# Optimization experiments

Measured on AMD Instinct MI355X. Metric: run time of the kernel, lower is better.

The kernel has to match this reference:

```python
import jax, jax.numpy as jnp
import numpy as np

BATCH, N, NX, NU, NY = 64, 4096, 128, 32, 32


def setup_inputs() -> dict:
    key = jax.random.key(0)
    k1, k2, k3, k4, k5 = jax.random.split(key, 5)
    # A scaled to spectral radius ~0.9 so the recurrence is stable (module has is_stable()).
    A = jax.random.normal(k1, (NX, NX), jnp.float32) * (0.9 / np.sqrt(NX).astype(np.float32))
    B = jax.random.normal(k2, (NX, NU), jnp.float32) * (1.0 / np.sqrt(NU).astype(np.float32))
    C = jax.random.normal(k3, (NY, NX), jnp.float32) * (1.0 / np.sqrt(NX).astype(np.float32))
    D = jax.random.normal(k4, (NY, NU), jnp.float32) * (1.0 / np.sqrt(NU).astype(np.float32))
    d = jax.random.normal(k5, (BATCH, N, NU, 1), jnp.float32)
    return {"d": d, "A": A, "B": B, "C": C, "D": D}


def reference(d, A, B, C, D):
    # d: [batch, N, nu, 1]. LTI recurrence: x_{k+1} = A x_k + B u_k ; y_k = C x_k + D u_k, x_0 = 0.
    u = jnp.swapaxes(d[..., 0], 0, 1)  # [N, batch, nu] time-major for scan
    x0 = jnp.zeros((d.shape[0], A.shape[0]), d.dtype)  # [batch, nx]

    def step(x, uk):
        y = x @ C.T + uk @ D.T          # [batch, ny] uses pre-update state x_k
        x_next = x @ A.T + uk @ B.T     # [batch, nx]
        return x_next, (y, x)

    xN, (ys, xs) = jax.lax.scan(step, x0, u)
    y = jnp.swapaxes(ys, 0, 1)[..., None]                      # [batch, N, ny, 1]
    x = jnp.swapaxes(xs, 0, 1)                                 # [batch, N, nx] = x_0..x_{N-1}
    x = jnp.concatenate([x, xN[:, None]], axis=1)[..., None]   # [batch, N+1, nx, 1]
    return y, (x,)
```

## Files before the change

### kernel.cpp

```cpp
#include <hip/hip_runtime.h>
#include <stdint.h>
#include <stddef.h>

typedef short s8v   __attribute__((ext_vector_type(8)));
typedef float f32x4 __attribute__((ext_vector_type(4)));

union BF8 { s8v v; unsigned short u[8]; };

__device__ __forceinline__ float bf16_f(unsigned short h) {
  unsigned u = ((unsigned)h) << 16;
  return __builtin_bit_cast(float, u);
}
__device__ __forceinline__ void split_trunc(float x, unsigned short &h, unsigned short &l) {
  unsigned u = __builtin_bit_cast(unsigned, x);
  h = (unsigned short)(u >> 16);
  float hi = __builtin_bit_cast(float, u & 0xFFFF0000u);
  float r = x - hi;
  l = (unsigned short)(__builtin_bit_cast(unsigned, r) >> 16);
}
__device__ __forceinline__ f32x4 mfma16(s8v a, s8v b, f32x4 c) {
  return __builtin_amdgcn_mfma_f32_16x16x32_bf16(a, b, c, 0, 0, 0);
}
__device__ __forceinline__ void split8(f32x4 a, f32x4 b, s8v &h, s8v &l) {
  BF8 hh, ll;
  #pragma unroll
  for (int i = 0; i < 4; ++i) { split_trunc(a[i], hh.u[i], ll.u[i]); split_trunc(b[i], hh.u[4 + i], ll.u[4 + i]); }
  h = hh.v; l = ll.v;
}

#define BATCH 64
#define NN    4096
#define NX    128
#define NU    32
#define NY    32
#define LPAD  132
#define CH    32
#define CPB   128

#define OFF_AH   0
#define OFF_AL   32768
#define OFF_BH   65536
#define OFF_BL   73728
#define OFF_CH   81920
#define OFF_CL   90112
#define OFF_DH   98304
#define OFF_DL   100352
#define OFF_A2H  102400
#define OFF_A2L  135168
#define OFF_ABH  167936
#define OFF_ABL  176128
#define OFF_G1H  184320
#define OFF_G1L  217088
#define OFF_G2H  249856
#define OFF_G2L  282624
#define OFF_G3H  315392
#define OFF_G3L  348160
#define OFF_P0   380928
#define OFF_P1   446464
#define OFF_V    512000
#define OFF_S    4706304
#define OFF_UH   8900608
#define OFF_UL   25677824

__global__ void k_prep(const float* __restrict__ A, const float* __restrict__ B,
                       const float* __restrict__ C, const float* __restrict__ D,
                       const float* __restrict__ d,
                       float* __restrict__ P, unsigned short* A2h, unsigned short* A2l,
                       unsigned short* Ah, unsigned short* Al,
                       unsigned short* Bh, unsigned short* Bl,
                       unsigned short* Ch, unsigned short* Cl,
                       unsigned short* Dh, unsigned short* Dl,
                       unsigned short* ABh, unsigned short* ABl,
                       unsigned short* Uh, unsigned short* Ul) {
  const int blk = blockIdx.x;
  if (blk >= 180) {
    const size_t i0 = ((size_t)(blk - 180) * 256 + threadIdx.x) * 8;
    f32x4 a = *(const f32x4*)(d + i0);
    f32x4 b = *(const f32x4*)(d + i0 + 4);
    s8v h, l; split8(a, b, h, l);
    *(s8v*)(Uh + i0) = h;
    *(s8v*)(Ul + i0) = l;
    return;
  }
  int gid = blk * 256 + threadIdx.x;
  if (blk < 64) {
    int row = gid >> 7, col = gid & 127;
    const float* xr = A + row * 128;
    float a0 = 0.f, a1 = 0.f;
    #pragma unroll 8
    for (int k = 0; k < 128; k += 2) {
      a0 = fmaf(xr[k],     A[k * 128 + col],       a0);
      a1 = fmaf(xr[k + 1], A[(k + 1) * 128 + col], a1);
    }
    float acc = a0 + a1;
    P[gid] = acc;
    unsigned short h, l; split_trunc(acc, h, l);
    A2h[gid] = h; A2l[gid] = l;
  } else if (blk < 164) {
    int idx = gid - 16384;
    unsigned short h, l;
    if (idx < 16384)      { split_trunc(A[idx], h, l); Ah[idx] = h; Al[idx] = l; }
    else if (idx < 20480) { int i = idx - 16384; split_trunc(B[i], h, l); Bh[i] = h; Bl[i] = l; }
    else if (idx < 24576) { int i = idx - 20480; split_trunc(C[i], h, l); Ch[i] = h; Cl[i] = l; }
    else if (idx < 25600) { int i = idx - 24576; split_trunc(D[i], h, l); Dh[i] = h; Dl[i] = l; }
  } else {
    int i = gid - 41984;
    int row = i >> 5, col = i & 31;
    float acc = 0.f;
    #pragma unroll 8
    for (int k = 0; k < 128; ++k) acc = fmaf(A[row * 128 + k], B[k * 32 + col], acc);
    unsigned short h, l; split_trunc(acc, h, l);
    ABh[i] = h; ABl[i] = l;
  }
}

__global__ void k_mm128(const float* __restrict__ X, const float* __restrict__ Y,
                        float* __restrict__ Z, unsigned short* Zh, unsigned short* Zl,
                        int writeBF) {
  int gid = blockIdx.x * 256 + threadIdx.x;
  int row = gid >> 7, col = gid & 127;
  const float* xr = X + row * 128;
  float a0 = 0.f, a1 = 0.f;
  #pragma unroll 8
  for (int k = 0; k < 128; k += 2) {
    a0 = fmaf(xr[k],     Y[k * 128 + col],       a0);
    a1 = fmaf(xr[k + 1], Y[(k + 1) * 128 + col], a1);
  }
  float acc = a0 + a1;
  Z[gid] = acc;
  if (writeBF) { unsigned short h, l; split_trunc(acc, h, l); Zh[gid] = h; Zl[gid] = l; }
}

__global__ __launch_bounds__(256, 2) void k_pass1(
    const unsigned short* __restrict__ Uh, const unsigned short* __restrict__ Ul,
    const unsigned short* __restrict__ A2h, const unsigned short* __restrict__ A2l,
    const unsigned short* __restrict__ ABh, const unsigned short* __restrict__ ABl,
    const unsigned short* __restrict__ Bh,  const unsigned short* __restrict__ Bl,
    float* __restrict__ vout) {
  __shared__ unsigned short Xh[2][16][LPAD];
  __shared__ unsigned short Xl[2][16][LPAD];
  const int tid = threadIdx.x;
  const int w = tid >> 6, l = tid & 63, q = l >> 4, m = l & 15;
  const int g = blockIdx.x;

  s8v fA2h[2][4], fA2l[2][4], fABh[2], fABl[2], fBh[2], fBl[2];
  #pragma unroll
  for (int t2 = 0; t2 < 2; ++t2) {
    const int n = (2 * w + t2) * 16 + m;
    #pragma unroll
    for (int kt = 0; kt < 4; ++kt) {
      const int k0 = kt * 32 + q * 8;
      fA2h[t2][kt] = *(const s8v*)(A2h + n * 128 + k0);
      fA2l[t2][kt] = *(const s8v*)(A2l + n * 128 + k0);
    }
    fABh[t2] = *(const s8v*)(ABh + n * 32 + q * 8);
    fABl[t2] = *(const s8v*)(ABl + n * 32 + q * 8);
    fBh[t2]  = *(const s8v*)(Bh  + n * 32 + q * 8);
    fBl[t2]  = *(const s8v*)(Bl  + n * 32 + q * 8);
  }
  for (int i = tid; i < 16 * LPAD; i += 256) {
    ((unsigned short*)Xh[0])[i] = 0;
    ((unsigned short*)Xl[0])[i] = 0;
  }
  __syncthreads();

  const int ch = g * 16 + m, b = ch >> 7, chunk = ch & (CPB - 1);
  const size_t ubase = ((size_t)b * NN + chunk * CH) * NU + q * 8;
  const unsigned short* uhb = Uh + ubase;
  const unsigned short* ulb = Ul + ubase;

  s8v u0h = *(const s8v*)(uhb),      u0l = *(const s8v*)(ulb);
  s8v u1h = *(const s8v*)(uhb + NU), u1l = *(const s8v*)(ulb + NU);

  f32x4 acc[2];
  #pragma unroll 2
  for (int r = 0; r < 16; ++r) {
    const int p = r & 1;
    s8v n0h = u0h, n0l = u0l, n1h = u1h, n1l = u1l;
    if (r < 15) {
      const size_t off = (size_t)(2 * r + 2) * NU;
      n0h = *(const s8v*)(uhb + off);      n0l = *(const s8v*)(ulb + off);
      n1h = *(const s8v*)(uhb + off + NU); n1l = *(const s8v*)(ulb + off + NU);
    }
    s8v fXh[4], fXl[4];
    #pragma unroll
    for (int kt = 0; kt < 4; ++kt) {
      fXh[kt] = *(const s8v*)&Xh[p][m][kt * 32 + q * 8];
      fXl[kt] = *(const s8v*)&Xl[p][m][kt * 32 + q * 8];
    }
    #pragma unroll
    for (int t2 = 0; t2 < 2; ++t2) {
      f32x4 a0 = {0.f,0.f,0.f,0.f}, a1 = {0.f,0.f,0.f,0.f}, a2 = {0.f,0.f,0.f,0.f};
      #pragma unroll
      for (int kt = 0; kt < 4; ++kt) a0 = mfma16(fXh[kt], fA2h[t2][kt], a0);
      a0 = mfma16(u0h, fABh[t2], a0);
      a0 = mfma16(u1h, fBh[t2],  a0);
      #pragma unroll
      for (int kt = 0; kt < 4; ++kt) a1 = mfma16(fXl[kt], fA2h[t2][kt], a1);
      a1 = mfma16(u0l, fABh[t2], a1);
      a1 = mfma16(u1l, fBh[t2],  a1);
      #pragma unroll
      for (int kt = 0; kt < 4; ++kt) a2 = mfma16(fXh[kt], fA2l[t2][kt], a2);
      a2 = mfma16(u0h, fABl[t2], a2);
      a2 = mfma16(u1h, fBl[t2],  a2);
      acc[t2] = a0 + a1 + a2;
    }
    if (r < 15) {
      #pragma unroll
      for (int t2 = 0; t2 < 2; ++t2) {
        const int col = (2 * w + t2) * 16 + m;
        #pragma unroll
        for (int rr = 0; rr < 4; ++rr) {
          unsigned short h, lo;
          split_trunc(acc[t2][rr], h, lo);
          Xh[1 - p][q * 4 + rr][col] = h;
          Xl[1 - p][q * 4 + rr][col] = lo;
        }
      }
      __syncthreads();
      u0h = n0h; u0l = n0l; u1h = n1h; u1l = n1l;
    }
  }
  #pragma unroll
  for (int t2 = 0; t2 < 2; ++t2) {
    const int col = (2 * w + t2) * 16 + m;
    #pragma unroll
    for (int rr = 0; rr < 4; ++rr) {
      const int row = g * 16 + q * 4 + rr;
      vout[(size_t)row * 128 + col] = acc[t2][rr];
    }
  }
}

__global__ __launch_bounds__(256, 2) void k_carry(
    const unsigned short* __restrict__ G1h, const unsigned short* __restrict__ G1l,
    const unsigned short* __restrict__ G2h, const unsigned short* __restrict__ G2l,
    const unsigned short* __restrict__ G3h, const unsigned short* __restrict__ G3l,
    const float* __restrict__ v, float* __restrict__ sout) {
  const int tid = threadIdx.x;
  const int w = tid >> 6, l = tid & 63, q = l >> 4, m = l & 15;
  const int g = blockIdx.x;
  const int chm = g * 16 + m, cm = chm & (CPB - 1);

  f32x4 a[2];
  a[0] = (f32x4){0.f,0.f,0.f,0.f};
  a[1] = (f32x4){0.f,0.f,0.f,0.f};

#define CARRY_TERM(GH, GL, DELTA)                                              \
  {                                                                            \
    const s8v zero = {0,0,0,0,0,0,0,0};                                        \
    s8v vh[4], vl[4];                                                          \
    _Pragma("unroll")                                                          \
    for (int kt = 0; kt < 4; ++kt) {                                           \
      if (cm >= DELTA) {                                                       \
        const float* vp = v + (size_t)(chm - DELTA) * NX + kt * 32 + q * 8;    \
        split8(*(const f32x4*)vp, *(const f32x4*)(vp + 4), vh[kt], vl[kt]);    \
      } else { vh[kt] = zero; vl[kt] = zero; }                                 \
    }                                                                          \
    _Pragma("unroll")                                                          \
    for (int t2 = 0; t2 < 2; ++t2) {                                           \
      const int n = (2 * w + t2) * 16 + m;                                     \
      _Pragma("unroll")                                                        \
      for (int kt = 0; kt < 4; ++kt) {                                         \
        const int k0 = kt * 32 + q * 8;                                        \
        s8v gh = *(const s8v*)(GH + n * NX + k0);                              \
        s8v gl = *(const s8v*)(GL + n * NX + k0);                              \
        a[t2] = mfma16(vh[kt], gh, a[t2]);                                     \
        a[t2] = mfma16(vl[kt], gh, a[t2]);                                     \
        a[t2] = mfma16(vh[kt], gl, a[t2]);                                     \
      }                                                                        \
    }                                                                          \
  }

  CARRY_TERM(G1h, G1l, 2)
  CARRY_TERM(G2h, G2l, 3)
  CARRY_TERM(G3h, G3l, 4)
#undef CARRY_TERM

  #pragma unroll
  for (int t2 = 0; t2 < 2; ++t2) {
    const int col = (2 * w + t2) * 16 + m;
    #pragma unroll
    for (int rr = 0; rr < 4; ++rr) {
      const int chr = g * 16 + q * 4 + rr, cr = chr & (CPB - 1);
      float sv = 0.f;
      if (cr >= 1) sv = a[t2][rr] + v[(size_t)(chr - 1) * NX + col];
      sout[(size_t)chr * NX + col] = sv;
    }
  }
}

__global__ __launch_bounds__(256, 2) void k_scan2(
    const unsigned short* __restrict__ Uh, const unsigned short* __restrict__ Ul,
    const float* __restrict__ s,
    const unsigned short* __restrict__ Ah, const unsigned short* __restrict__ Al,
    const unsigned short* __restrict__ Bh, const unsigned short* __restrict__ Bl,
    const unsigned short* __restrict__ Ch, const unsigned short* __restrict__ Cl,
    const unsigned short* __restrict__ Dh, const unsigned short* __restrict__ Dl,
    float* __restrict__ yout, float* __restrict__ xout) {
  __shared__ unsigned short Eh[16][LPAD];
  __shared__ unsigned short El[16][LPAD];
  __shared__ unsigned short Oh[16][LPAD];
  __shared__ unsigned short Ol[16][LPAD];
  const int tid = threadIdx.x;
  const int w = tid >> 6, l = tid & 63, q = l >> 4, m = l & 15;
  const int g = blockIdx.x;

  s8v fAh[2][4], fAl[2][4], fBh[2], fBl[2];
  #pragma unroll
  for (int t2 = 0; t2 < 2; ++t2) {
    const int n = (2 * w + t2) * 16 + m;
    #pragma unroll
    for (int kt = 0; kt < 4; ++kt) {
      const int k0 = kt * 32 + q * 8;
      fAh[t2][kt] = *(const s8v*)(Ah + n * 128 + k0);
      fAl[t2][kt] = *(const s8v*)(Al + n * 128 + k0);
    }
    fBh[t2] = *(const s8v*)(Bh + n * 32 + q * 8);
    fBl[t2] = *(const s8v*)(Bl + n * 32 + q * 8);
  }
  s8v fCh[4], fCl[4], fDh, fDl;
  {
    const int o = (w & 1) * 16 + m;
    #pragma unroll
    for (int kt = 0; kt < 4; ++kt) {
      const int k0 = kt * 32 + q * 8;
      fCh[kt] = *(const s8v*)(Ch + o * 128 + k0);
      fCl[kt] = *(const s8v*)(Cl + o * 128 + k0);
    }
    fDh = *(const s8v*)(Dh + o * 32 + q * 8);
    fDl = *(const s8v*)(Dl + o * 32 + q * 8);
  }

  {
    const int lb = tid >> 4, i0 = (tid & 15) * 8;
    const int chS = g * 16 + lb, bS = chS >> 7, cS = chS & (CPB - 1);
    const float* sp = s + (size_t)chS * 128 + i0;
    f32x4 s0 = *(const f32x4*)sp, s1 = *(const f32x4*)(sp + 4);
    s8v hh, ll;
    split8(s0, s1, hh, ll);
    *(s8v*)&Eh[lb][i0] = hh;
    *(s8v*)&El[lb][i0] = ll;
    float* xp = xout + ((size_t)bS * (NN + 1) + (size_t)cS * CH) * NX + i0;
    *(f32x4*)xp = s0;
    *(f32x4*)(xp + 4) = s1;
  }
  __syncthreads();

  const int ch = g * 16 + m, b = ch >> 7, chunk = ch & (CPB - 1);
  const size_t ubase = ((size_t)b * NN + chunk * CH) * NU + q * 8;
  const unsigned short* uhb = Uh + ubase;
  const unsigned short* ulb = Ul + ubase;

  float* xptr[2][4];
  bool xlast[2][4];
  float* yptr[4];
  #pragma unroll
  for (int t2 = 0; t2 < 2; ++t2) {
    const int col = (2 * w + t2) * 16 + m;
    #pragma unroll
    for (int rr = 0; rr < 4; ++rr) {
      const int chX = g * 16 + q * 4 + rr, bX = chX >> 7, cX = chX & (CPB - 1);
      xptr[t2][rr] = xout + ((size_t)bX * (NN + 1) + (size_t)cX * CH + 1) * NX + col;
      xlast[t2][rr] = (cX == CPB - 1);
    }
  }
  #pragma unroll
  for (int rr = 0; rr < 4; ++rr) {
    const int chY = g * 16 + q * 4 + rr, bY = chY >> 7, cY = chY & (CPB - 1);
    yptr[rr] = yout + ((size_t)bY * NN + (size_t)cY * CH) * NY + (w & 1) * 16 + m;
  }

  s8v u0h = *(const s8v*)(uhb),      u0l = *(const s8v*)(ulb);
  s8v u1h = *(const s8v*)(uhb + NU), u1l = *(const s8v*)(ulb + NU);

  #pragma unroll 1
  for (int r = 0; r < 16; ++r) {
    s8v n0h = u0h, n0l = u0l, n1h = u1h, n1l = u1l;
    if (r < 15) {
      const size_t off = (size_t)(2 * r + 2) * NU;
      n0h = *(const s8v*)(uhb + off);      n0l = *(const s8v*)(ulb + off);
      n1h = *(const s8v*)(uhb + off + NU); n1l = *(const s8v*)(ulb + off + NU);
    }
    s8v fXh[4], fXl[4];
    #pragma unroll
    for (int kt = 0; kt < 4; ++kt) {
      fXh[kt] = *(const s8v*)&Eh[m][kt * 32 + q * 8];
      fXl[kt] = *(const s8v*)&El[m][kt * 32 + q * 8];
    }
    f32x4 xo[2];
    #pragma unroll
    for (int t2 = 0; t2 < 2; ++t2) {
      f32x4 a0 = {0.f,0.f,0.f,0.f}, a1 = {0.f,0.f,0.f,0.f}, a2 = {0.f,0.f,0.f,0.f};
      #pragma unroll
      for (int kt = 0; kt < 4; ++kt) a0 = mfma16(fXh[kt], fAh[t2][kt], a0);
      a0 = mfma16(u0h, fBh[t2], a0);
      #pragma unroll
      for (int kt = 0; kt < 4; ++kt) a1 = mfma16(fXl[kt], fAh[t2][kt], a1);
      a1 = mfma16(u0l, fBh[t2], a1);
      #pragma unroll
      for (int kt = 0; kt < 4; ++kt) a2 = mfma16(fXh[kt], fAl[t2][kt], a2);
      a2 = mfma16(u0h, fBl[t2], a2);
      xo[t2] = a0 + a1 + a2;
    }
    if (w < 2) {
      f32x4 b0 = {0.f,0.f,0.f,0.f}, b1 = {0.f,0.f,0.f,0.f}, b2 = {0.f,0.f,0.f,0.f};
      #pragma unroll
      for (int kt = 0; kt < 4; ++kt) b0 = mfma16(fXh[kt], fCh[kt], b0);
      b0 = mfma16(u0h, fDh, b0);
      #pragma unroll
      for (int kt = 0; kt < 4; ++kt) b1 = mfma16(fXl[kt], fCh[kt], b1);
      b1 = mfma16(u0l, fDh, b1);
      #pragma unroll
      for (int kt = 0; kt < 4; ++kt) b2 = mfma16(fXh[kt], fCl[kt], b2);
      b2 = mfma16(u0h, fDl, b2);
      f32x4 yv = b0 + b1 + b2;
      #pragma unroll
      for (int rr = 0; rr < 4; ++rr) *(yptr[rr]) = yv[rr];
    }
    #pragma unroll
    for (int t2 = 0; t2 < 2; ++t2) {
      const int col = (2 * w + t2) * 16 + m;
      #pragma unroll
      for (int rr = 0; rr < 4; ++rr) {
        *(xptr[t2][rr]) = xo[t2][rr];
        unsigned short h, lo;
        split_trunc(xo[t2][rr], h, lo);
        Oh[q * 4 + rr][col] = h;
        Ol[q * 4 + rr][col] = lo;
      }
    }
    __syncthreads();

    s8v fOh[4], fOl[4];
    #pragma unroll
    for (int kt = 0; kt < 4; ++kt) {
      fOh[kt] = *(const s8v*)&Oh[m][kt * 32 + q * 8];
      fOl[kt] = *(const s8v*)&Ol[m][kt * 32 + q * 8];
    }
    f32x4 xe[2];
    #pragma unroll
    for (int t2 = 0; t2 < 2; ++t2) {
      f32x4 a0 = {0.f,0.f,0.f,0.f}, a1 = {0.f,0.f,0.f,0.f}, a2 = {0.f,0.f,0.f,0.f};
      #pragma unroll
      for (int kt = 0; kt < 4; ++kt) a0 = mfma16(fOh[kt], fAh[t2][kt], a0);
      a0 = mfma16(u1h, fBh[t2], a0);
      #pragma unroll
      for (int kt = 0; kt < 4; ++kt) a1 = mfma16(fOl[kt], fAh[t2][kt], a1);
      a1 = mfma16(u1l, fBh[t2], a1);
      #pragma unroll
      for (int kt = 0; kt < 4; ++kt) a2 = mfma16(fOh[kt], fAl[t2][kt], a2);
      a2 = mfma16(u1h, fBl[t2], a2);
      xe[t2] = a0 + a1 + a2;
    }
    if (w >= 2) {
      f32x4 c0 = {0.f,0.f,0.f,0.f}, c1 = {0.f,0.f,0.f,0.f}, c2 = {0.f,0.f,0.f,0.f};
      #pragma unroll
      for (int kt = 0; kt < 4; ++kt) c0 = mfma16(fOh[kt], fCh[kt], c0);
      c0 = mfma16(u1h, fDh, c0);
      #pragma unroll
      for (int kt = 0; kt < 4; ++kt) c1 = mfma16(fOl[kt], fCh[kt], c1);
      c1 = mfma16(u1l, fDh, c1);
      #pragma unroll
      for (int kt = 0; kt < 4; ++kt) c2 = mfma16(fOh[kt], fCl[kt], c2);
      c2 = mfma16(u1h, fDl, c2);
      f32x4 yv = c0 + c1 + c2;
      #pragma unroll
      for (int rr = 0; rr < 4; ++rr) *(yptr[rr] + NY) = yv[rr];
    }
    #pragma unroll
    for (int t2 = 0; t2 < 2; ++t2) {
      const int col = (2 * w + t2) * 16 + m;
      #pragma unroll
      for (int rr = 0; rr < 4; ++rr) {
        if (r < 15 || xlast[t2][rr]) *(xptr[t2][rr] + NX) = xe[t2][rr];
        unsigned short h, lo;
        split_trunc(xe[t2][rr], h, lo);
        Eh[q * 4 + rr][col] = h;
        El[q * 4 + rr][col] = lo;
      }
    }
    __syncthreads();

    if (r < 15) {
      u0h = n0h; u0l = n0l; u1h = n1h; u1l = n1l;
      #pragma unroll
      for (int t2 = 0; t2 < 2; ++t2)
        #pragma unroll
        for (int rr = 0; rr < 4; ++rr) xptr[t2][rr] += 2 * NX;
      #pragma unroll
      for (int rr = 0; rr < 4; ++rr) yptr[rr] += 2 * NY;
    }
  }
}

extern "C" void kernel_launch(void* const* d_in, const int* in_sizes, int n_in,
                              void* d_out, int out_size, void* d_ws, size_t ws_size,
                              hipStream_t stream) {
  (void)in_sizes; (void)n_in; (void)out_size; (void)ws_size;
  const float* d = (const float*)d_in[0];
  const float* A = (const float*)d_in[1];
  const float* B = (const float*)d_in[2];
  const float* C = (const float*)d_in[3];
  const float* D = (const float*)d_in[4];

  char* ws = (char*)d_ws;
  unsigned short* Ah  = (unsigned short*)(ws + OFF_AH);
  unsigned short* Al  = (unsigned short*)(ws + OFF_AL);
  unsigned short* Bh  = (unsigned short*)(ws + OFF_BH);
  unsigned short* Bl  = (unsigned short*)(ws + OFF_BL);
  unsigned short* Chp = (unsigned short*)(ws + OFF_CH);
  unsigned short* Clp = (unsigned short*)(ws + OFF_CL);
  unsigned short* Dhp = (unsigned short*)(ws + OFF_DH);
  unsigned short* Dlp = (unsigned short*)(ws + OFF_DL);
  unsigned short* A2h = (unsigned short*)(ws + OFF_A2H);
  unsigned short* A2l = (unsigned short*)(ws + OFF_A2L);
  unsigned short* ABh = (unsigned short*)(ws + OFF_ABH);
  unsigned short* ABl = (unsigned short*)(ws + OFF_ABL);
  unsigned short* G1h = (unsigned short*)(ws + OFF_G1H);
  unsigned short* G1l = (unsigned short*)(ws + OFF_G1L);
  unsigned short* G2h = (unsigned short*)(ws + OFF_G2H);
  unsigned short* G2l = (unsigned short*)(ws + OFF_G2L);
  unsigned short* G3h = (unsigned short*)(ws + OFF_G3H);
  unsigned short* G3l = (unsigned short*)(ws + OFF_G3L);
  unsigned short* Uh  = (unsigned short*)(ws + OFF_UH);
  unsigned short* Ul  = (unsigned short*)(ws + OFF_UL);
  float* P0 = (float*)(ws + OFF_P0);
  float* P1 = (float*)(ws + OFF_P1);
  float* V  = (float*)(ws + OFF_V);
  float* S  = (float*)(ws + OFF_S);

  float* yout = (float*)d_out;
  float* xout = yout + (size_t)BATCH * NN * NY;

  k_prep<<<4276, 256, 0, stream>>>(A, B, C, D, d, P0, A2h, A2l,
                                   Ah, Al, Bh, Bl, Chp, Clp, Dhp, Dlp,
                                   ABh, ABl, Uh, Ul);
  k_mm128<<<64, 256, 0, stream>>>(P0, P0, P1, nullptr, nullptr, 0);
  k_mm128<<<64, 256, 0, stream>>>(P1, P1, P0, nullptr, nullptr, 0);
  k_mm128<<<64, 256, 0, stream>>>(P0, P0, P1, nullptr, nullptr, 0);
  k_mm128<<<64, 256, 0, stream>>>(P1, P1, P0, G1h, G1l, 1);
  k_mm128<<<64, 256, 0, stream>>>(P0, P0, P1, G2h, G2l, 1);
  k_mm128<<<64, 256, 0, stream>>>(P0, P1, V,  G3h, G3l, 1);

  k_pass1<<<512, 256, 0, stream>>>(Uh, Ul, A2h, A2l, ABh, ABl, Bh, Bl, V);
  k_carry<<<512, 256, 0, stream>>>(G1h, G1l, G2h, G2l, G3h, G3l, V, S);
  k_scan2<<<512, 256, 0, stream>>>(Uh, Ul, S, Ah, Al, Bh, Bl, Chp, Clp, Dhp, Dlp,
                                   yout, xout);
}
```

Baseline: 295.0 us.

## Replace serial chunk recurrence with impulse-response GEMM and cooperative constant kernel

The chunk-local state pass no longer steps through the recurrence within each 32-step chunk. It builds the impulse-response matrix K = [A^31 B … A B, B] once and computes each chunk's end state as a single GEMM of the chunk inputs against K, using split bf16 MFMA. The matrix powers and K are computed in one cooperative-groups kernel with grid syncs in place of six separate matmul launches. This removes the serialized dependency chain and per-step syncthreads from pass1 and cuts launch overhead. The cost is extra work to build K and the reliance on cooperative launch with only 64 blocks.

```diff
diff --git a/kernel.cpp b/kernel.cpp
--- a/kernel.cpp
+++ b/kernel.cpp
@@ -1,4 +1,5 @@
 #include <hip/hip_runtime.h>
+#include <hip/hip_cooperative_groups.h>
 #include <stdint.h>
 #include <stddef.h>
 
@@ -7,10 +8,6 @@
 
 union BF8 { s8v v; unsigned short u[8]; };
 
-__device__ __forceinline__ float bf16_f(unsigned short h) {
-  unsigned u = ((unsigned)h) << 16;
-  return __builtin_bit_cast(float, u);
-}
 __device__ __forceinline__ void split_trunc(float x, unsigned short &h, unsigned short &l) {
   unsigned u = __builtin_bit_cast(unsigned, x);
   h = (unsigned short)(u >> 16);
@@ -41,40 +38,36 @@
 #define OFF_AL   32768
 #define OFF_BH   65536
 #define OFF_BL   73728
-#define OFF_CH   81920
-#define OFF_CL   90112
+#define OFF_CHS  81920
+#define OFF_CLS  90112
 #define OFF_DH   98304
 #define OFF_DL   100352
-#define OFF_A2H  102400
-#define OFF_A2L  135168
-#define OFF_ABH  167936
-#define OFF_ABL  176128
-#define OFF_G1H  184320
-#define OFF_G1L  217088
-#define OFF_G2H  249856
-#define OFF_G2L  282624
-#define OFF_G3H  315392
-#define OFF_G3L  348160
-#define OFF_P0   380928
-#define OFF_P1   446464
-#define OFF_V    512000
-#define OFF_S    4706304
-#define OFF_UH   8900608
-#define OFF_UL   25677824
+#define OFF_G1H  102400
+#define OFF_G1L  135168
+#define OFF_G2H  167936
+#define OFF_G2L  200704
+#define OFF_G3H  233472
+#define OFF_G3L  266240
+#define OFF_V    299008
+#define OFF_S    4493312
+#define OFF_UH   8687616
+#define OFF_UL   25464832
+#define OFF_KH   42242048
+#define OFF_KL   42504192
+#define OFF_S5   42766336
+#define OFF_PW   43290624
 
 __global__ void k_prep(const float* __restrict__ A, const float* __restrict__ B,
                        const float* __restrict__ C, const float* __restrict__ D,
                        const float* __restrict__ d,
-                       float* __restrict__ P, unsigned short* A2h, unsigned short* A2l,
                        unsigned short* Ah, unsigned short* Al,
                        unsigned short* Bh, unsigned short* Bl,
                        unsigned short* Ch, unsigned short* Cl,
                        unsigned short* Dh, unsigned short* Dl,
-                       unsigned short* ABh, unsigned short* ABl,
                        unsigned short* Uh, unsigned short* Ul) {
   const int blk = blockIdx.x;
-  if (blk >= 180) {
-    const size_t i0 = ((size_t)(blk - 180) * 256 + threadIdx.x) * 8;
+  if (blk >= 100) {
+    const size_t i0 = ((size_t)(blk - 100) * 256 + threadIdx.x) * 8;
     f32x4 a = *(const f32x4*)(d + i0);
     f32x4 b = *(const f32x4*)(d + i0 + 4);
     s8v h, l; split8(a, b, h, l);
@@ -82,153 +75,129 @@
     *(s8v*)(Ul + i0) = l;
     return;
   }
-  int gid = blk * 256 + threadIdx.x;
-  if (blk < 64) {
+  int idx = blk * 256 + threadIdx.x;
+  unsigned short h, l;
+  if (idx < 16384)      { split_trunc(A[idx], h, l); Ah[idx] = h; Al[idx] = l; }
+  else if (idx < 20480) { int i = idx - 16384; split_trunc(B[i], h, l); Bh[i] = h; Bl[i] = l; }
+  else if (idx < 24576) { int i = idx - 20480; split_trunc(C[i], h, l); Ch[i] = h; Cl[i] = l; }
+  else if (idx < 25600) { int i = idx - 24576; split_trunc(D[i], h, l); Dh[i] = h; Dl[i] = l; }
+}
+
+__global__ __launch_bounds__(256) void k_const(
+    const float* __restrict__ A, const float* __restrict__ B,
+    float* __restrict__ PW, float* __restrict__ S,
+    unsigned short* G1h, unsigned short* G1l,
+    unsigned short* G2h, unsigned short* G2l,
+    unsigned short* G3h, unsigned short* G3l,
+    unsigned short* Kh, unsigned short* Kl) {
+  cooperative_groups::grid_group grid = cooperative_groups::this_grid();
+  const int gid = blockIdx.x * 256 + threadIdx.x;
+  float* A2  = PW;
+  float* A4  = PW + 16384;
+  float* A8  = PW + 32768;
+  float* A16 = PW + 49152;
+  float* A32 = PW + 65536;
+  float* A64 = PW + 81920;
+  float* A96 = PW + 98304;
+
+  auto mm = [&](const float* X, const float* Y, float* Z) {
     int row = gid >> 7, col = gid & 127;
-    const float* xr = A + row * 128;
+    const float* xr = X + row * 128;
     float a0 = 0.f, a1 = 0.f;
     #pragma unroll 8
     for (int k = 0; k < 128; k += 2) {
-      a0 = fmaf(xr[k],     A[k * 128 + col],       a0);
-      a1 = fmaf(xr[k + 1], A[(k + 1) * 128 + col], a1);
-    }
-    float acc = a0 + a1;
-    P[gid] = acc;
-    unsigned short h, l; split_trunc(acc, h, l);
-    A2h[gid] = h; A2l[gid] = l;
-  } else if (blk < 164) {
-    int idx = gid - 16384;
+      a0 = fmaf(xr[k],     Y[k * 128 + col],       a0);
+      a1 = fmaf(xr[k + 1], Y[(k + 1) * 128 + col], a1);
+    }
+    Z[gid] = a0 + a1;
+  };
+  auto sstep = [&](const float* Ap, int half, int sh) {
+    for (int idx = gid; idx < 128 * half; idx += 16384) {
+      int i = idx >> sh, c = idx & (half - 1);
+      const float* ar = Ap + i * 128;
+      float acc = 0.f;
+      #pragma unroll 8
+      for (int k = 0; k < 128; ++k) acc = fmaf(ar[k], S[k * 1024 + c], acc);
+      S[i * 1024 + half + c] = acc;
+    }
+  };
+  auto splitbuf = [&](const float* src, unsigned short* dh, unsigned short* dl) {
     unsigned short h, l;
-    if (idx < 16384)      { split_trunc(A[idx], h, l); Ah[idx] = h; Al[idx] = l; }
-    else if (idx < 20480) { int i = idx - 16384; split_trunc(B[i], h, l); Bh[i] = h; Bl[i] = l; }
-    else if (idx < 24576) { int i = idx - 20480; split_trunc(C[i], h, l); Ch[i] = h; Cl[i] = l; }
-    else if (idx < 25600) { int i = idx - 24576; split_trunc(D[i], h, l); Dh[i] = h; Dl[i] = l; }
-  } else {
-    int i = gid - 41984;
-    int row = i >> 5, col = i & 31;
+    split_trunc(src[gid], h, l);
+    dh[gid] = h; dl[gid] = l;
+  };
+
+  mm(A, A, A2);
+  if (gid < 4096) {
+    int i = gid >> 5, j = gid & 31;
+    S[i * 1024 + j] = B[gid];
     float acc = 0.f;
     #pragma unroll 8
-    for (int k = 0; k < 128; ++k) acc = fmaf(A[row * 128 + k], B[k * 32 + col], acc);
-    unsigned short h, l; split_trunc(acc, h, l);
-    ABh[i] = h; ABl[i] = l;
-  }
-}
-
-__global__ void k_mm128(const float* __restrict__ X, const float* __restrict__ Y,
-                        float* __restrict__ Z, unsigned short* Zh, unsigned short* Zl,
-                        int writeBF) {
-  int gid = blockIdx.x * 256 + threadIdx.x;
-  int row = gid >> 7, col = gid & 127;
-  const float* xr = X + row * 128;
-  float a0 = 0.f, a1 = 0.f;
-  #pragma unroll 8
-  for (int k = 0; k < 128; k += 2) {
-    a0 = fmaf(xr[k],     Y[k * 128 + col],       a0);
-    a1 = fmaf(xr[k + 1], Y[(k + 1) * 128 + col], a1);
-  }
-  float acc = a0 + a1;
-  Z[gid] = acc;
-  if (writeBF) { unsigned short h, l; split_trunc(acc, h, l); Zh[gid] = h; Zl[gid] = l; }
-}
-
-__global__ __launch_bounds__(256, 2) void k_pass1(
+    for (int k = 0; k < 128; ++k) acc = fmaf(A[i * 128 + k], B[k * 32 + j], acc);
+    S[i * 1024 + 32 + j] = acc;
+  }
+  grid.sync();
+  mm(A2, A2, A4);   sstep(A2, 64, 6);    grid.sync();
+  mm(A4, A4, A8);   sstep(A4, 128, 7);   grid.sync();
+  mm(A8, A8, A16);  sstep(A8, 256, 8);   grid.sync();
+  mm(A16, A16, A32); sstep(A16, 512, 9); grid.sync();
+  mm(A32, A32, A64);
+  splitbuf(A32, G1h, G1l);
+  for (int idx = gid; idx < 131072; idx += 16384) {
+    int i = idx >> 10, kk = idx & 1023;
+    int t = kk >> 5, j = kk & 31;
+    unsigned short h, l;
+    split_trunc(S[i * 1024 + (31 - t) * 32 + j], h, l);
+    Kh[idx] = h; Kl[idx] = l;
+  }
+  grid.sync();
+  mm(A64, A32, A96);
+  splitbuf(A64, G2h, G2l);
+  grid.sync();
+  splitbuf(A96, G3h, G3l);
+}
+
+__global__ __launch_bounds__(256, 4) void k_vgemm(
     const unsigned short* __restrict__ Uh, const unsigned short* __restrict__ Ul,
-    const unsigned short* __restrict__ A2h, const unsigned short* __restrict__ A2l,
-    const unsigned short* __restrict__ ABh, const unsigned short* __restrict__ ABl,
-    const unsigned short* __restrict__ Bh,  const unsigned short* __restrict__ Bl,
+    const unsigned short* __restrict__ Kh, const unsigned short* __restrict__ Kl,
     float* __restrict__ vout) {
-  __shared__ unsigned short Xh[2][16][LPAD];
-  __shared__ unsigned short Xl[2][16][LPAD];
   const int tid = threadIdx.x;
   const int w = tid >> 6, l = tid & 63, q = l >> 4, m = l & 15;
   const int g = blockIdx.x;
-
-  s8v fA2h[2][4], fA2l[2][4], fABh[2], fABl[2], fBh[2], fBl[2];
-  #pragma unroll
-  for (int t2 = 0; t2 < 2; ++t2) {
-    const int n = (2 * w + t2) * 16 + m;
-    #pragma unroll
-    for (int kt = 0; kt < 4; ++kt) {
-      const int k0 = kt * 32 + q * 8;
-      fA2h[t2][kt] = *(const s8v*)(A2h + n * 128 + k0);
-      fA2l[t2][kt] = *(const s8v*)(A2l + n * 128 + k0);
-    }
-    fABh[t2] = *(const s8v*)(ABh + n * 32 + q * 8);
-    fABl[t2] = *(const s8v*)(ABl + n * 32 + q * 8);
-    fBh[t2]  = *(const s8v*)(Bh  + n * 32 + q * 8);
-    fBl[t2]  = *(const s8v*)(Bl  + n * 32 + q * 8);
-  }
-  for (int i = tid; i < 16 * LPAD; i += 256) {
-    ((unsigned short*)Xh[0])[i] = 0;
-    ((unsigned short*)Xl[0])[i] = 0;
-  }
-  __syncthreads();
-
   const int ch = g * 16 + m, b = ch >> 7, chunk = ch & (CPB - 1);
   const size_t ubase = ((size_t)b * NN + chunk * CH) * NU + q * 8;
   const unsigned short* uhb = Uh + ubase;
   const unsigned short* ulb = Ul + ubase;
-
-  s8v u0h = *(const s8v*)(uhb),      u0l = *(const s8v*)(ulb);
-  s8v u1h = *(const s8v*)(uhb + NU), u1l = *(const s8v*)(ulb + NU);
-
-  f32x4 acc[2];
-  #pragma unroll 2
-  for (int r = 0; r < 16; ++r) {
-    const int p = r & 1;
-    s8v n0h = u0h, n0l = u0l, n1h = u1h, n1l = u1l;
-    if (r < 15) {
-      const size_t off = (size_t)(2 * r + 2) * NU;
-      n0h = *(const s8v*)(uhb + off);      n0l = *(const s8v*)(ulb + off);
-      n1h = *(const s8v*)(uhb + off + NU); n1l = *(const s8v*)(ulb + off + NU);
-    }
-    s8v fXh[4], fXl[4];
-    #pragma unroll
-    for (int kt = 0; kt < 4; ++kt) {
-      fXh[kt] = *(const s8v*)&Xh[p][m][kt * 32 + q * 8];
-      fXl[kt] = *(const s8v*)&Xl[p][m][kt * 32 + q * 8];
-    }
-    #pragma unroll
-    for (int t2 = 0; t2 < 2; ++t2) {
-      f32x4 a0 = {0.f,0.f,0.f,0.f}, a1 = {0.f,0.f,0.f,0.f}, a2 = {0.f,0.f,0.f,0.f};
-      #pragma unroll
-      for (int kt = 0; kt < 4; ++kt) a0 = mfma16(fXh[kt], fA2h[t2][kt], a0);
-      a0 = mfma16(u0h, fABh[t2], a0);
-      a0 = mfma16(u1h, fBh[t2],  a0);
-      #pragma unroll
-      for (int kt = 0; kt < 4; ++kt) a1 = mfma16(fXl[kt], fA2h[t2][kt], a1);
-      a1 = mfma16(u0l, fABh[t2], a1);
-      a1 = mfma16(u1l, fBh[t2],  a1);
-      #pragma unroll
-      for (int kt = 0; kt < 4; ++kt) a2 = mfma16(fXh[kt], fA2l[t2][kt], a2);
-      a2 = mfma16(u0h, fABl[t2], a2);
-      a2 = mfma16(u1h, fBl[t2],  a2);
-      acc[t2] = a0 + a1 + a2;
-    }
-    if (r < 15) {
-      #pragma unroll
-      for (int t2 = 0; t2 < 2; ++t2) {
-        const int col = (2 * w + t2) * 16 + m;
-        #pragma unroll
-        for (int rr = 0; rr < 4; ++rr) {
-          unsigned short h, lo;
-          split_trunc(acc[t2][rr], h, lo);
-          Xh[1 - p][q * 4 + rr][col] = h;
-          Xl[1 - p][q * 4 + rr][col] = lo;
-        }
-      }
-      __syncthreads();
-      u0h = n0h; u0l = n0l; u1h = n1h; u1l = n1l;
-    }
-  }
+  const int n0 = (2 * w) * 16 + m, n1 = (2 * w + 1) * 16 + m;
+  const unsigned short* kh0 = Kh + n0 * 1024 + q * 8;
+  const unsigned short* kl0 = Kl + n0 * 1024 + q * 8;
+  const unsigned short* kh1 = Kh + n1 * 1024 + q * 8;
+  const unsigned short* kl1 = Kl + n1 * 1024 + q * 8;
+
+  f32x4 a00 = {0,0,0,0}, a01 = {0,0,0,0}, a02 = {0,0,0,0};
+  f32x4 a10 = {0,0,0,0}, a11 = {0,0,0,0}, a12 = {0,0,0,0};
+  #pragma unroll 4
+  for (int t = 0; t < 32; ++t) {
+    s8v uh  = *(const s8v*)(uhb + t * 32);
+    s8v ul  = *(const s8v*)(ulb + t * 32);
+    s8v k0h = *(const s8v*)(kh0 + t * 32);
+    s8v k0l = *(const s8v*)(kl0 + t * 32);
+    s8v k1h = *(const s8v*)(kh1 + t * 32);
+    s8v k1l = *(const s8v*)(kl1 + t * 32);
+    a00 = mfma16(uh, k0h, a00);
+    a01 = mfma16(ul, k0h, a01);
+    a02 = mfma16(uh, k0l, a02);
+    a10 = mfma16(uh, k1h, a10);
+    a11 = mfma16(ul, k1h, a11);
+    a12 = mfma16(uh, k1l, a12);
+  }
+  f32x4 acc0 = a00 + a01 + a02;
+  f32x4 acc1 = a10 + a11 + a12;
   #pragma unroll
-  for (int t2 = 0; t2 < 2; ++t2) {
-    const int col = (2 * w + t2) * 16 + m;
-    #pragma unroll
-    for (int rr = 0; rr < 4; ++rr) {
-      const int row = g * 16 + q * 4 + rr;
-      vout[(size_t)row * 128 + col] = acc[t2][rr];
-    }
+  for (int rr = 0; rr < 4; ++rr) {
+    const int row = g * 16 + q * 4 + rr;
+    vout[(size_t)row * 128 + n0] = acc0[rr];
+    vout[(size_t)row * 128 + n1] = acc1[rr];
   }
 }
 
@@ -509,14 +478,10 @@
   unsigned short* Al  = (unsigned short*)(ws + OFF_AL);
   unsigned short* Bh  = (unsigned short*)(ws + OFF_BH);
   unsigned short* Bl  = (unsigned short*)(ws + OFF_BL);
-  unsigned short* Chp = (unsigned short*)(ws + OFF_CH);
-  unsigned short* Clp = (unsigned short*)(ws + OFF_CL);
+  unsigned short* Chp = (unsigned short*)(ws + OFF_CHS);
+  unsigned short* Clp = (unsigned short*)(ws + OFF_CLS);
   unsigned short* Dhp = (unsigned short*)(ws + OFF_DH);
   unsigned short* Dlp = (unsigned short*)(ws + OFF_DL);
-  unsigned short* A2h = (unsigned short*)(ws + OFF_A2H);
-  unsigned short* A2l = (unsigned short*)(ws + OFF_A2L);
-  unsigned short* ABh = (unsigned short*)(ws + OFF_ABH);
-  unsigned short* ABl = (unsigned short*)(ws + OFF_ABL);
   unsigned short* G1h = (unsigned short*)(ws + OFF_G1H);
   unsigned short* G1l = (unsigned short*)(ws + OFF_G1L);
   unsigned short* G2h = (unsigned short*)(ws + OFF_G2H);
@@ -525,25 +490,26 @@
   unsigned short* G3l = (unsigned short*)(ws + OFF_G3L);
   unsigned short* Uh  = (unsigned short*)(ws + OFF_UH);
   unsigned short* Ul  = (unsigned short*)(ws + OFF_UL);
-  float* P0 = (float*)(ws + OFF_P0);
-  float* P1 = (float*)(ws + OFF_P1);
+  unsigned short* Kh  = (unsigned short*)(ws + OFF_KH);
+  unsigned short* Kl  = (unsigned short*)(ws + OFF_KL);
+  float* S5 = (float*)(ws + OFF_S5);
+  float* PW = (float*)(ws + OFF_PW);
   float* V  = (float*)(ws + OFF_V);
   float* S  = (float*)(ws + OFF_S);
 
   float* yout = (float*)d_out;
   float* xout = yout + (size_t)BATCH * NN * NY;
 
-  k_prep<<<4276, 256, 0, stream>>>(A, B, C, D, d, P0, A2h, A2l,
-                                   Ah, Al, Bh, Bl, Chp, Clp, Dhp, Dlp,
-                                   ABh, ABl, Uh, Ul);
-  k_mm128<<<64, 256, 0, stream>>>(P0, P0, P1, nullptr, nullptr, 0);
-  k_mm128<<<64, 256, 0, stream>>>(P1, P1, P0, nullptr, nullptr, 0);
-  k_mm128<<<64, 256, 0, stream>>>(P0, P0, P1, nullptr, nullptr, 0);
-  k_mm128<<<64, 256, 0, stream>>>(P1, P1, P0, G1h, G1l, 1);
-  k_mm128<<<64, 256, 0, stream>>>(P0, P0, P1, G2h, G2l, 1);
-  k_mm128<<<64, 256, 0, stream>>>(P0, P1, V,  G3h, G3l, 1);
-
-  k_pass1<<<512, 256, 0, stream>>>(Uh, Ul, A2h, A2l, ABh, ABl, Bh, Bl, V);
+  k_prep<<<4196, 256, 0, stream>>>(A, B, C, D, d,
+                                   Ah, Al, Bh, Bl, Chp, Clp, Dhp, Dlp, Uh, Ul);
+
+  void* cargs[] = {(void*)&A, (void*)&B, (void*)&PW, (void*)&S5,
+                   (void*)&G1h, (void*)&G1l, (void*)&G2h, (void*)&G2l,
+                   (void*)&G3h, (void*)&G3l, (void*)&Kh, (void*)&Kl};
+  hipLaunchCooperativeKernel((const void*)k_const, dim3(64), dim3(256),
+                             cargs, 0u, stream);
+
+  k_vgemm<<<512, 256, 0, stream>>>(Uh, Ul, Kh, Kl, V);
   k_carry<<<512, 256, 0, stream>>>(G1h, G1l, G2h, G2l, G3h, G3l, V, S);
   k_scan2<<<512, 256, 0, stream>>>(Uh, Ul, S, Ah, Al, Bh, Bl, Chp, Clp, Dhp, Dlp,
                                    yout, xout);
```

Result: slower. 430.4 us (+45.9%).
